# Performance work log

Hardware: AMD Instinct MI355X
Metric: run time of the kernel (lower is better)

## Reference

```python
import jax, jax.numpy as jnp
import numpy as np

B, NX, NR, D, H = 8, 512, 512, 256, 256


def setup_inputs() -> dict:
    key = jax.random.key(0)
    ks = jax.random.split(key, 8)
    s = 1.0 / np.sqrt(D)
    sh = 1.0 / np.sqrt(H)
    return {
        "X": jax.random.normal(ks[0], (B, NX, D), dtype=jnp.float32),
        "ref": jax.random.normal(ks[1], (B, NR, D), dtype=jnp.float32),
        "W_X": jax.random.normal(ks[2], (H, D), dtype=jnp.float32) * s,
        "b_X": jax.random.normal(ks[3], (H,), dtype=jnp.float32) * s,
        "W_ref": jax.random.normal(ks[4], (H, D), dtype=jnp.float32) * s,
        "b_ref": jax.random.normal(ks[5], (H,), dtype=jnp.float32) * s,
        "v_w": jax.random.normal(ks[6], (1, H), dtype=jnp.float32) * sh,
        "v_b": jax.random.normal(ks[7], (1,), dtype=jnp.float32) * sh,
    }


def reference(X, ref, W_X, b_X, W_ref, b_ref, v_w, v_b):
    # linear projections: [B, nX, H], [B, nR, H]
    hX = jnp.einsum('bxd,hd->bxh', X, W_X) + b_X
    hR = jnp.einsum('brd,hd->brh', ref, W_ref) + b_ref
    # additive (Bahdanau) scores: [B, nX, nR]
    t = jnp.tanh(hX[:, :, None, :] + hR[:, None, :, :])
    out = jnp.einsum('bxrh,h->bxr', t, v_w[0]) + v_b[0]
    # softmax over the n_X axis (dim=1 in torch)
    attn = jax.nn.softmax(out, axis=1)
    # weighted sum of X per ref position: [B, nR, D]
    weighted_X = jnp.einsum('bxe,bxr->bre', X, attn)
    return weighted_X
```

## Files before the change

kernel.cpp:

```cpp
#include <hip/hip_runtime.h>
#include <math.h>

#define CB 8
#define CNX 512
#define CNR 512
#define CD 256
#define CH 256

__device__ __forceinline__ float fast_rcp(float x) {
#if __has_builtin(__builtin_amdgcn_rcpf)
  return __builtin_amdgcn_rcpf(x);
#else
  return 1.0f / x;
#endif
}
__device__ __forceinline__ float fast_exp2(float x) {
#if __has_builtin(__builtin_amdgcn_exp2f)
  return __builtin_amdgcn_exp2f(x);
#else
  return exp2f(x);
#endif
}

__global__ __launch_bounds__(256) void proj_fused(
    const float* __restrict__ A0, const float* __restrict__ A1,
    const float* __restrict__ W0, const float* __restrict__ W1,
    const float* __restrict__ bias0, const float* __restrict__ bias1,
    float* __restrict__ E0, float* __restrict__ E1) {
  __shared__ float As[16][68];
  __shared__ float Ws[16][68];
  const int K = CD;
  int z = blockIdx.z;
  const float* A = z ? A1 : A0;
  const float* W = z ? W1 : W0;
  const float* bias = z ? bias1 : bias0;
  float* ET = z ? E1 : E0;
  int m0 = blockIdx.x * 64, n0 = blockIdx.y * 64;
  int tid = threadIdx.x;
  int tx = tid & 15, ty = tid >> 4;
  int lrow = tid >> 2, lc4 = tid & 3;
  float acc[4][4] = {};
  const float* pA = A + (size_t)(m0 + lrow) * K + lc4 * 4;
  const float* pW = W + (size_t)(n0 + lrow) * K + lc4 * 4;
  for (int kt = 0; kt < K; kt += 16) {
    float4 av = *(const float4*)(pA + kt);
    float4 wv = *(const float4*)(pW + kt);
    __syncthreads();
    As[lc4 * 4 + 0][lrow] = av.x;
    As[lc4 * 4 + 1][lrow] = av.y;
    As[lc4 * 4 + 2][lrow] = av.z;
    As[lc4 * 4 + 3][lrow] = av.w;
    Ws[lc4 * 4 + 0][lrow] = wv.x;
    Ws[lc4 * 4 + 1][lrow] = wv.y;
    Ws[lc4 * 4 + 2][lrow] = wv.z;
    Ws[lc4 * 4 + 3][lrow] = wv.w;
    __syncthreads();
#pragma unroll
    for (int k = 0; k < 16; k++) {
      float4 a4 = *(const float4*)&As[k][ty * 4];
      float4 w4 = *(const float4*)&Ws[k][tx * 4];
      float am[4] = {a4.x, a4.y, a4.z, a4.w};
      float wm[4] = {w4.x, w4.y, w4.z, w4.w};
#pragma unroll
      for (int i = 0; i < 4; i++)
#pragma unroll
        for (int j = 0; j < 4; j++)
          acc[i][j] = fmaf(am[i], wm[j], acc[i][j]);
    }
  }
  const float K2L = 2.8853900817779268f;
  float4 bv = *(const float4*)(bias + n0 + tx * 4);
  float bm[4] = {bv.x, bv.y, bv.z, bv.w};
  int b = m0 >> 9;
  int xbase = (m0 & 511) + ty * 4;
#pragma unroll
  for (int j = 0; j < 4; j++) {
    int h = n0 + tx * 4 + j;
    float4 o = {fast_exp2(K2L * (acc[0][j] + bm[j])),
                fast_exp2(K2L * (acc[1][j] + bm[j])),
                fast_exp2(K2L * (acc[2][j] + bm[j])),
                fast_exp2(K2L * (acc[3][j] + bm[j]))};
    *(float4*)(ET + ((size_t)b * CH + h) * CNX + xbase) = o;
  }
}

__global__ __launch_bounds__(256) void scores_kernel(
    const float* __restrict__ exT, const float* __restrict__ erT,
    const float* __restrict__ v_w, float* __restrict__ scT) {
  __shared__ float xs[64][32];
  __shared__ float rs[64][32];
  __shared__ float vsh[CH];
  int b = blockIdx.z;
  int x0 = blockIdx.x * 32, r0 = blockIdx.y * 32;
  int tid = threadIdx.x;
  int tx = tid & 15, ty = tid >> 4;
  vsh[tid] = v_w[tid];
  float acc[2][2] = {};
  const float* pX = exT + (size_t)b * CH * CNX + x0;
  const float* pR = erT + (size_t)b * CH * CNR + r0;
  int srow = tid >> 3, sc4 = tid & 7;
  for (int hc = 0; hc < CH; hc += 64) {
    float4 xv0 = *(const float4*)(pX + (size_t)(hc + srow) * CNX + sc4 * 4);
    float4 xv1 = *(const float4*)(pX + (size_t)(hc + srow + 32) * CNX + sc4 * 4);
    float4 rv0 = *(const float4*)(pR + (size_t)(hc + srow) * CNR + sc4 * 4);
    float4 rv1 = *(const float4*)(pR + (size_t)(hc + srow + 32) * CNR + sc4 * 4);
    __syncthreads();
    *(float4*)&xs[srow][sc4 * 4] = xv0;
    *(float4*)&xs[srow + 32][sc4 * 4] = xv1;
    *(float4*)&rs[srow][sc4 * 4] = rv0;
    *(float4*)&rs[srow + 32][sc4 * 4] = rv1;
    __syncthreads();
#pragma unroll 4
    for (int hq = 0; hq < 16; hq++) {
      int h0 = hq * 4;
      float4 vv = *(const float4*)&vsh[hc + h0];
      float2 xa = *(const float2*)&xs[h0 + 0][tx * 2];
      float2 xb = *(const float2*)&xs[h0 + 1][tx * 2];
      float2 xc = *(const float2*)&xs[h0 + 2][tx * 2];
      float2 xd = *(const float2*)&xs[h0 + 3][tx * 2];
      float2 ra = *(const float2*)&rs[h0 + 0][ty * 2];
      float2 rb = *(const float2*)&rs[h0 + 1][ty * 2];
      float2 rc = *(const float2*)&rs[h0 + 2][ty * 2];
      float2 rd = *(const float2*)&rs[h0 + 3][ty * 2];
      float xam[2] = {xa.x, xa.y}, xbm[2] = {xb.x, xb.y};
      float xcm[2] = {xc.x, xc.y}, xdm[2] = {xd.x, xd.y};
      float ram[2] = {ra.x, ra.y}, rbm[2] = {rb.x, rb.y};
      float rcm[2] = {rc.x, rc.y}, rdm[2] = {rd.x, rd.y};
#pragma unroll
      for (int i = 0; i < 2; i++)
#pragma unroll
        for (int j = 0; j < 2; j++) {
          float a = fmaf(ram[i], xam[j], 1.0f);
          float bb = fmaf(rbm[i], xbm[j], 1.0f);
          float c = fmaf(rcm[i], xcm[j], 1.0f);
          float d = fmaf(rdm[i], xdm[j], 1.0f);
          float q12 = a * bb, q34 = c * d;
          float p12 = fmaf(vv.y, a, vv.x * bb);
          float p34 = fmaf(vv.w, c, vv.z * d);
          float num = fmaf(p34, q12, p12 * q34);
          acc[i][j] = fmaf(num, fast_rcp(q12 * q34), acc[i][j]);
        }
    }
  }
  float* pO = scT + ((size_t)b * CNR + r0 + ty * 2) * CNX + x0 + tx * 2;
#pragma unroll
  for (int i = 0; i < 2; i++) {
    float2 o = {-2.0f * acc[i][0], -2.0f * acc[i][1]};
    *(float2*)(pO + (size_t)i * CNX) = o;
  }
}

__global__ __launch_bounds__(256) void wsum_fused(
    const float* __restrict__ scT, const float* __restrict__ X,
    float* __restrict__ out) {
  __shared__ float As[32][33];
  __shared__ float Bs[32][68];
  __shared__ float dn[32];
  const float L2E = 1.4426950408889634f;
  int b = blockIdx.z;
  int r0 = blockIdx.x * 32, d0 = blockIdx.y * 64;
  int tid = threadIdx.x;
  int tx = tid & 15, ty = tid >> 4;
  int arow = tid >> 3, ak4 = tid & 7;
  int brow = tid >> 4, bc4 = tid & 15;
  float acc[2][4] = {};
  float dsum = 0.0f;
  for (int kt = 0; kt < CNX; kt += 32) {
    float4 sv = *(const float4*)(scT + ((size_t)b * CNR + r0 + arow) * CNX + kt + ak4 * 4);
    float4 ev = {fast_exp2(sv.x * L2E), fast_exp2(sv.y * L2E),
                 fast_exp2(sv.z * L2E), fast_exp2(sv.w * L2E)};
    dsum += (ev.x + ev.y) + (ev.z + ev.w);
    float4 bv0 = *(const float4*)(X + ((size_t)b * CNX + kt + brow) * CD + d0 + bc4 * 4);
    float4 bv1 = *(const float4*)(X + ((size_t)b * CNX + kt + brow + 16) * CD + d0 + bc4 * 4);
    __syncthreads();
    As[ak4 * 4 + 0][arow] = ev.x;
    As[ak4 * 4 + 1][arow] = ev.y;
    As[ak4 * 4 + 2][arow] = ev.z;
    As[ak4 * 4 + 3][arow] = ev.w;
    *(float4*)&Bs[brow][bc4 * 4] = bv0;
    *(float4*)&Bs[brow + 16][bc4 * 4] = bv1;
    __syncthreads();
#pragma unroll 8
    for (int k = 0; k < 32; k++) {
      float a0 = As[k][ty * 2], a1 = As[k][ty * 2 + 1];
      float4 b4 = *(const float4*)&Bs[k][tx * 4];
      float bm[4] = {b4.x, b4.y, b4.z, b4.w};
#pragma unroll
      for (int j = 0; j < 4; j++) {
        acc[0][j] = fmaf(a0, bm[j], acc[0][j]);
        acc[1][j] = fmaf(a1, bm[j], acc[1][j]);
      }
    }
  }
  dsum += __shfl_xor(dsum, 1, 64);
  dsum += __shfl_xor(dsum, 2, 64);
  dsum += __shfl_xor(dsum, 4, 64);
  if ((tid & 7) == 0) dn[arow] = dsum;
  __syncthreads();
  float inv0 = fast_rcp(dn[ty * 2]);
  float inv1 = fast_rcp(dn[ty * 2 + 1]);
  float* pO = out + ((size_t)b * CNR + r0 + ty * 2) * CD + d0 + tx * 4;
  float4 o0 = {acc[0][0] * inv0, acc[0][1] * inv0, acc[0][2] * inv0, acc[0][3] * inv0};
  float4 o1 = {acc[1][0] * inv1, acc[1][1] * inv1, acc[1][2] * inv1, acc[1][3] * inv1};
  *(float4*)(pO) = o0;
  *(float4*)(pO + CD) = o1;
}

extern "C" void kernel_launch(void* const* d_in, const int* in_sizes, int n_in,
                              void* d_out, int out_size, void* d_ws, size_t ws_size,
                              hipStream_t stream) {
  const float* X     = (const float*)d_in[0];
  const float* ref   = (const float*)d_in[1];
  const float* W_X   = (const float*)d_in[2];
  const float* b_X   = (const float*)d_in[3];
  const float* W_ref = (const float*)d_in[4];
  const float* b_ref = (const float*)d_in[5];
  const float* v_w   = (const float*)d_in[6];
  float* out = (float*)d_out;
  float* ws  = (float*)d_ws;

  float* exT = ws;
  float* erT = ws + 1048576;
  float* scT = ws + 2097152;

  proj_fused<<<dim3(64, 4, 2), 256, 0, stream>>>(X, ref, W_X, W_ref, b_X, b_ref, exT, erT);
  scores_kernel<<<dim3(16, 16, 8), 256, 0, stream>>>(exT, erT, v_w, scT);
  wsum_fused<<<dim3(16, 4, 8), 256, 0, stream>>>(scT, X, out);
}
```

Baseline: 161.5 us.

## Widen scores tile to 64 x-columns and move softmax exp into scores epilogue

```diff
diff --git a/kernel.cpp b/kernel.cpp
--- a/kernel.cpp
+++ b/kernel.cpp
@@ -86,50 +86,60 @@
 
 __global__ __launch_bounds__(256) void scores_kernel(
     const float* __restrict__ exT, const float* __restrict__ erT,
-    const float* __restrict__ v_w, float* __restrict__ scT) {
-  __shared__ float xs[64][32];
+    const float* __restrict__ v_w, float* __restrict__ eT) {
+  __shared__ float xs[64][64];
   __shared__ float rs[64][32];
   __shared__ float vsh[CH];
   int b = blockIdx.z;
-  int x0 = blockIdx.x * 32, r0 = blockIdx.y * 32;
+  int x0 = blockIdx.x * 64, r0 = blockIdx.y * 32;
   int tid = threadIdx.x;
   int tx = tid & 15, ty = tid >> 4;
   vsh[tid] = v_w[tid];
-  float acc[2][2] = {};
+  float acc[2][4] = {};
   const float* pX = exT + (size_t)b * CH * CNX + x0;
   const float* pR = erT + (size_t)b * CH * CNR + r0;
-  int srow = tid >> 3, sc4 = tid & 7;
+  int xrow = tid >> 4, xc4 = tid & 15;
+  int rrow = tid >> 3, rc4 = tid & 7;
   for (int hc = 0; hc < CH; hc += 64) {
-    float4 xv0 = *(const float4*)(pX + (size_t)(hc + srow) * CNX + sc4 * 4);
-    float4 xv1 = *(const float4*)(pX + (size_t)(hc + srow + 32) * CNX + sc4 * 4);
-    float4 rv0 = *(const float4*)(pR + (size_t)(hc + srow) * CNR + sc4 * 4);
-    float4 rv1 = *(const float4*)(pR + (size_t)(hc + srow + 32) * CNR + sc4 * 4);
-    __syncthreads();
-    *(float4*)&xs[srow][sc4 * 4] = xv0;
-    *(float4*)&xs[srow + 32][sc4 * 4] = xv1;
-    *(float4*)&rs[srow][sc4 * 4] = rv0;
-    *(float4*)&rs[srow + 32][sc4 * 4] = rv1;
+    float4 xv[4], rv[2];
+#pragma unroll
+    for (int p = 0; p < 4; p++)
+      xv[p] = *(const float4*)(pX + (size_t)(hc + xrow + p * 16) * CNX + xc4 * 4);
+#pragma unroll
+    for (int p = 0; p < 2; p++)
+      rv[p] = *(const float4*)(pR + (size_t)(hc + rrow + p * 32) * CNR + rc4 * 4);
+    __syncthreads();
+#pragma unroll
+    for (int p = 0; p < 4; p++)
+      *(float4*)&xs[xrow + p * 16][xc4 * 4] = xv[p];
+#pragma unroll
+    for (int p = 0; p < 2; p++)
+      *(float4*)&rs[rrow + p * 32][rc4 * 4] = rv[p];
     __syncthreads();
 #pragma unroll 4
     for (int hq = 0; hq < 16; hq++) {
       int h0 = hq * 4;
       float4 vv = *(const float4*)&vsh[hc + h0];
-      float2 xa = *(const float2*)&xs[h0 + 0][tx * 2];
-      float2 xb = *(const float2*)&xs[h0 + 1][tx * 2];
-      float2 xc = *(const float2*)&xs[h0 + 2][tx * 2];
-      float2 xd = *(const float2*)&xs[h0 + 3][tx * 2];
+      float4 xa = *(const float4*)&xs[h0 + 0][tx * 4];
+      float4 xb = *(const float4*)&xs[h0 + 1][tx * 4];
+      float4 xc = *(const float4*)&xs[h0 + 2][tx * 4];
+      float4 xd = *(const float4*)&xs[h0 + 3][tx * 4];
       float2 ra = *(const float2*)&rs[h0 + 0][ty * 2];
       float2 rb = *(const float2*)&rs[h0 + 1][ty * 2];
       float2 rc = *(const float2*)&rs[h0 + 2][ty * 2];
       float2 rd = *(const float2*)&rs[h0 + 3][ty * 2];
-      float xam[2] = {xa.x, xa.y}, xbm[2] = {xb.x, xb.y};
-      float xcm[2] = {xc.x, xc.y}, xdm[2] = {xd.x, xd.y};
-      float ram[2] = {ra.x, ra.y}, rbm[2] = {rb.x, rb.y};
-      float rcm[2] = {rc.x, rc.y}, rdm[2] = {rd.x, rd.y};
+      float xam[4] = {xa.x, xa.y, xa.z, xa.w};
+      float xbm[4] = {xb.x, xb.y, xb.z, xb.w};
+      float xcm[4] = {xc.x, xc.y, xc.z, xc.w};
+      float xdm[4] = {xd.x, xd.y, xd.z, xd.w};
+      float ram[2] = {ra.x, ra.y};
+      float rbm[2] = {rb.x, rb.y};
+      float rcm[2] = {rc.x, rc.y};
+      float rdm[2] = {rd.x, rd.y};
 #pragma unroll
       for (int i = 0; i < 2; i++)
 #pragma unroll
-        for (int j = 0; j < 2; j++) {
+        for (int j = 0; j < 4; j++) {
           float a = fmaf(ram[i], xam[j], 1.0f);
           float bb = fmaf(rbm[i], xbm[j], 1.0f);
           float c = fmaf(rcm[i], xcm[j], 1.0f);
@@ -142,21 +152,22 @@
         }
     }
   }
-  float* pO = scT + ((size_t)b * CNR + r0 + ty * 2) * CNX + x0 + tx * 2;
+  const float NL2E = -2.0f * 1.4426950408889634f;
+  float* pO = eT + ((size_t)b * CNR + r0 + ty * 2) * CNX + x0 + tx * 4;
 #pragma unroll
   for (int i = 0; i < 2; i++) {
-    float2 o = {-2.0f * acc[i][0], -2.0f * acc[i][1]};
-    *(float2*)(pO + (size_t)i * CNX) = o;
+    float4 o = {fast_exp2(acc[i][0] * NL2E), fast_exp2(acc[i][1] * NL2E),
+                fast_exp2(acc[i][2] * NL2E), fast_exp2(acc[i][3] * NL2E)};
+    *(float4*)(pO + (size_t)i * CNX) = o;
   }
 }
 
 __global__ __launch_bounds__(256) void wsum_fused(
-    const float* __restrict__ scT, const float* __restrict__ X,
+    const float* __restrict__ eT, const float* __restrict__ X,
     float* __restrict__ out) {
-  __shared__ float As[32][33];
+  __shared__ float As[32][34];
   __shared__ float Bs[32][68];
   __shared__ float dn[32];
-  const float L2E = 1.4426950408889634f;
   int b = blockIdx.z;
   int r0 = blockIdx.x * 32, d0 = blockIdx.y * 64;
   int tid = threadIdx.x;
@@ -166,9 +177,7 @@
   float acc[2][4] = {};
   float dsum = 0.0f;
   for (int kt = 0; kt < CNX; kt += 32) {
-    float4 sv = *(const float4*)(scT + ((size_t)b * CNR + r0 + arow) * CNX + kt + ak4 * 4);
-    float4 ev = {fast_exp2(sv.x * L2E), fast_exp2(sv.y * L2E),
-                 fast_exp2(sv.z * L2E), fast_exp2(sv.w * L2E)};
+    float4 ev = *(const float4*)(eT + ((size_t)b * CNR + r0 + arow) * CNX + kt + ak4 * 4);
     dsum += (ev.x + ev.y) + (ev.z + ev.w);
     float4 bv0 = *(const float4*)(X + ((size_t)b * CNX + kt + brow) * CD + d0 + bc4 * 4);
     float4 bv1 = *(const float4*)(X + ((size_t)b * CNX + kt + brow + 16) * CD + d0 + bc4 * 4);
@@ -182,13 +191,13 @@
     __syncthreads();
 #pragma unroll 8
     for (int k = 0; k < 32; k++) {
-      float a0 = As[k][ty * 2], a1 = As[k][ty * 2 + 1];
+      float2 a2 = *(const float2*)&As[k][ty * 2];
       float4 b4 = *(const float4*)&Bs[k][tx * 4];
       float bm[4] = {b4.x, b4.y, b4.z, b4.w};
 #pragma unroll
       for (int j = 0; j < 4; j++) {
-        acc[0][j] = fmaf(a0, bm[j], acc[0][j]);
-        acc[1][j] = fmaf(a1, bm[j], acc[1][j]);
+        acc[0][j] = fmaf(a2.x, bm[j], acc[0][j]);
+        acc[1][j] = fmaf(a2.y, bm[j], acc[1][j]);
       }
     }
   }
@@ -221,9 +230,9 @@
 
   float* exT = ws;
   float* erT = ws + 1048576;
-  float* scT = ws + 2097152;
+  float* eT  = ws + 2097152;
 
   proj_fused<<<dim3(64, 4, 2), 256, 0, stream>>>(X, ref, W_X, W_ref, b_X, b_ref, exT, erT);
-  scores_kernel<<<dim3(16, 16, 8), 256, 0, stream>>>(exT, erT, v_w, scT);
-  wsum_fused<<<dim3(16, 4, 8), 256, 0, stream>>>(scT, X, out);
-}
+  scores_kernel<<<dim3(8, 16, 8), 256, 0, stream>>>(exT, erT, v_w, eT);
+  wsum_fused<<<dim3(16, 4, 8), 256, 0, stream>>>(eT, X, out);
+}
```

After: 176.3 us. 9.2% more time.
